# Kernel tuning notes

Hardware: AMD Instinct MI355X
Metric: run time of the kernel (lower is better)

## Reference

```python
import jax, jax.numpy as jnp
import numpy as np
import math

B, S, HID = 2, 2048, 2048
NH, NKV = 32, 8
HD = HID // NH  # 64
N_REP = NH // NKV  # 4


def setup_inputs() -> dict:
    key = jax.random.key(0)
    ks = jax.random.split(key, 7)
    sc = 0.02
    return {
        "hidden_states": jax.random.normal(ks[0], (B, S, HID), jnp.float32),
        "cos": jax.random.normal(ks[1], (S, HD), jnp.float32),
        "sin": jax.random.normal(ks[2], (S, HD), jnp.float32),
        "wq": jax.random.normal(ks[3], (NH * HD, HID), jnp.float32) * sc,
        "wk": jax.random.normal(ks[4], (NKV * HD, HID), jnp.float32) * sc,
        "wv": jax.random.normal(ks[5], (NKV * HD, HID), jnp.float32) * sc,
        "wo": jax.random.normal(ks[6], (HID, NH * HD), jnp.float32) * sc,
    }


def _rotate_half(x):
    x1, x2 = jnp.split(x, 2, axis=-1)
    return jnp.concatenate([-x2, x1], axis=-1)


def _apply_rotary(q, k, cos, sin):
    # q: [B,S,NH,HD], k: [B,S,NKV,HD]; cos/sin: [S,HD] broadcast over batch, heads
    c = cos[None, :, None, :]
    s = sin[None, :, None, :]
    return q * c + _rotate_half(q) * s, k * c + _rotate_half(k) * s


def reference(hidden_states, cos, sin, wq, wk, wv, wo):
    x = hidden_states  # [B,S,HID]
    q = jnp.einsum('bsh,dh->bsd', x, wq).reshape(B, S, NH, HD)
    k = jnp.einsum('bsh,dh->bsd', x, wk).reshape(B, S, NKV, HD)
    v = jnp.einsum('bsh,dh->bsd', x, wv).reshape(B, S, NKV, HD)
    q, k = _apply_rotary(q, k, cos, sin)
    # repeat_kv: expand kv heads by N_REP -> [B,S,NH,HD]
    k = jnp.repeat(k, N_REP, axis=2)
    v = jnp.repeat(v, N_REP, axis=2)
    # [B,NH,S,HD]
    q = q.transpose(0, 2, 1, 3)
    k = k.transpose(0, 2, 1, 3)
    v = v.transpose(0, 2, 1, 3)
    scores = jnp.einsum('bhqd,bhkd->bhqk', q, k) / math.sqrt(HD)
    probs = jax.nn.softmax(scores.astype(jnp.float32), axis=-1).astype(q.dtype)
    out = jnp.einsum('bhqk,bhkd->bhqd', probs, v)
    out = out.transpose(0, 2, 1, 3).reshape(B, S, NH * HD)
    return jnp.einsum('bsd,hd->bsh', out, wo)
```

## Files before the change

### kernel.cpp

```cpp
#include <hip/hip_runtime.h>
#include <math.h>

#define B 2
#define S 2048
#define HID 2048
#define NH 32
#define NKV 8
#define HD 64
#define NREP 4

typedef __bf16 bf16_t;
typedef bf16_t bf16x8 __attribute__((ext_vector_type(8)));
typedef bf16_t bf16x4 __attribute__((ext_vector_type(4)));
typedef bf16_t bf16x2 __attribute__((ext_vector_type(2)));
typedef float floatx4 __attribute__((ext_vector_type(4)));

__device__ __forceinline__ void gld_lds16(const void* g, void* l) {
    __builtin_amdgcn_global_load_lds(
        (const __attribute__((address_space(1))) void*)g,
        (__attribute__((address_space(3))) void*)l, 16, 0, 0);
}

__device__ __forceinline__ int pack2(float a, float b) {
    bf16x2 v; v[0] = (bf16_t)a; v[1] = (bf16_t)b;
    return __builtin_bit_cast(int, v);
}

__device__ __forceinline__ bf16x8 cat8i(int2 lo, int2 hi) {
    int4 w; w.x = lo.x; w.y = lo.y; w.z = hi.x; w.w = hi.y;
    return __builtin_bit_cast(bf16x8, w);
}

__global__ __launch_bounds__(256) void cast_all(const float* __restrict__ x,
                                                const float* __restrict__ wq,
                                                const float* __restrict__ wk,
                                                const float* __restrict__ wv,
                                                const float* __restrict__ wo,
                                                bf16_t* __restrict__ xb,
                                                bf16_t* __restrict__ wqkvb,
                                                bf16_t* __restrict__ wob) {
    int gid = blockIdx.x * 256 + threadIdx.x;
    const float* src; bf16_t* dst; int idx;
    if (gid < 1048576)      { src = x;  dst = xb;               idx = gid; }
    else if (gid < 1572864) { src = wq; dst = wqkvb;            idx = gid - 1048576; }
    else if (gid < 1703936) { src = wk; dst = wqkvb + 4194304;  idx = gid - 1572864; }
    else if (gid < 1835008) { src = wv; dst = wqkvb + 5242880;  idx = gid - 1703936; }
    else                    { src = wo; dst = wob;              idx = gid - 1835008; }
    size_t i = (size_t)idx * 8;
    float4 f0 = *(const float4*)(src + i);
    float4 f1 = *(const float4*)(src + i + 4);
    bf16x8 v;
    v[0] = (bf16_t)f0.x; v[1] = (bf16_t)f0.y; v[2] = (bf16_t)f0.z; v[3] = (bf16_t)f0.w;
    v[4] = (bf16_t)f1.x; v[5] = (bf16_t)f1.y; v[6] = (bf16_t)f1.z; v[7] = (bf16_t)f1.w;
    *(bf16x8*)(dst + i) = v;
}

#define TM 128
#define TN 128
#define BK 64

enum { MODE_QKV = 0, MODE_OUT = 2 };

template <int MODE>
__global__ __launch_bounds__(256) void gemm_mfma(const bf16_t* __restrict__ A,
                                                 const bf16_t* __restrict__ W,
                                                 void* __restrict__ outQ,
                                                 bf16_t* __restrict__ outK,
                                                 bf16_t* __restrict__ outV,
                                                 const float* __restrict__ cosp,
                                                 const float* __restrict__ sinp,
                                                 int M, int N, int K) {
    __shared__ __align__(16) bf16_t As[2 * TM * 32];
    __shared__ __align__(16) bf16_t Ws[2 * TN * 32];
    const int t    = threadIdx.x;
    const int wave = t >> 6, lane = t & 63;
    const int quad = lane >> 4, l16 = lane & 15;
    const int m0 = blockIdx.y * TM, n0 = blockIdx.x * TN;
    const int wm = (wave >> 1) * 64, wn = (wave & 1) * 64;

    floatx4 zero4 = {0.f, 0.f, 0.f, 0.f};
    floatx4 acc[4][4];
    #pragma unroll
    for (int i = 0; i < 4; ++i)
        #pragma unroll
        for (int j = 0; j < 4; ++j) acc[i][j] = zero4;

    const int r4 = t >> 2;
    const int c8 = (t & 3) * 8;
    const bf16_t* Arow = A + (size_t)(m0 + r4) * K + c8;
    const bf16_t* Wrow = W + (size_t)(n0 + r4) * K + c8;

    for (int k0 = 0; k0 < K; k0 += BK) {
        #pragma unroll
        for (int ks = 0; ks < 2; ++ks) {
            gld_lds16(Arow + k0 + ks * 32,          As + ks * 4096 + t * 8);
            gld_lds16(Arow + 64 * K + k0 + ks * 32, As + ks * 4096 + 2048 + t * 8);
            gld_lds16(Wrow + k0 + ks * 32,          Ws + ks * 4096 + t * 8);
            gld_lds16(Wrow + 64 * K + k0 + ks * 32, Ws + ks * 4096 + 2048 + t * 8);
        }
        __syncthreads();
        #pragma unroll
        for (int ks = 0; ks < 2; ++ks) {
            bf16x8 af[4], bfr[4];
            #pragma unroll
            for (int i = 0; i < 4; ++i)
                af[i] = *(bf16x8*)&As[ks * 4096 + (wm + i * 16 + l16) * 32 + quad * 8];
            #pragma unroll
            for (int j = 0; j < 4; ++j)
                bfr[j] = *(bf16x8*)&Ws[ks * 4096 + (wn + j * 16 + l16) * 32 + quad * 8];
            #pragma unroll
            for (int i = 0; i < 4; ++i)
                #pragma unroll
                for (int j = 0; j < 4; ++j)
                    acc[i][j] = __builtin_amdgcn_mfma_f32_16x16x32_bf16(af[i], bfr[j], acc[i][j], 0, 0, 0);
        }
        __syncthreads();
    }

    if constexpr (MODE == MODE_OUT) {
        float* C = (float*)outQ;
        #pragma unroll
        for (int i = 0; i < 4; ++i)
            #pragma unroll
            for (int r = 0; r < 4; ++r) {
                int row = m0 + wm + i * 16 + quad * 4 + r;
                #pragma unroll
                for (int j = 0; j < 4; ++j)
                    C[(size_t)row * N + n0 + wn + j * 16 + l16] = acc[i][j][r];
            }
    } else {
        const int hh = (n0 + wn) / 64;
        #pragma unroll
        for (int i = 0; i < 4; ++i)
            #pragma unroll
            for (int r = 0; r < 4; ++r) {
                int m = m0 + wm + i * 16 + quad * 4 + r;
                int b = m / S, s = m % S;
                if (hh < NH + NKV) {
                    bf16_t* base;
                    float sc;
                    if (hh < NH) {
                        base = (bf16_t*)outQ + ((size_t)(b * NH + hh) * S + s) * HD;
                        sc = 0.18033688011f;
                    } else {
                        base = outK + ((size_t)(b * NKV + (hh - NH)) * S + s) * HD;
                        sc = 1.0f;
                    }
                    #pragma unroll
                    for (int j = 0; j < 2; ++j) {
                        int d = j * 16 + l16;
                        float x1 = acc[i][j][r], x2 = acc[i][j + 2][r];
                        float c1 = cosp[s * HD + d],      s1 = sinp[s * HD + d];
                        float c2 = cosp[s * HD + d + 32], s2 = sinp[s * HD + d + 32];
                        base[d]      = (bf16_t)((x1 * c1 - x2 * s1) * sc);
                        base[d + 32] = (bf16_t)((x2 * c2 + x1 * s2) * sc);
                    }
                } else {
                    int kvh = hh - NH - NKV;
                    int w  = s & 63, lo = w & 31;
                    int pos = (lo < 16) ? (((lo >> 2) << 3) | (lo & 3))
                                        : ((((lo - 16) >> 2) << 3) | 4 | (lo & 3));
                    int ps = (s & ~63) | ((w & 32) + pos);
                    bf16_t* vb = outV + ((size_t)(b * NKV + kvh) * HD) * S + ps;
                    #pragma unroll
                    for (int j = 0; j < 4; ++j)
                        vb[(size_t)(j * 16 + l16) * S] = (bf16_t)acc[i][j][r];
                }
            }
    }
}

__global__ __launch_bounds__(256, 4) void attn_mfma(const bf16_t* __restrict__ Q,
                                                    const bf16_t* __restrict__ Kb,
                                                    const bf16_t* __restrict__ Vt,
                                                    bf16_t* __restrict__ Ob) {
    __shared__ __align__(16) bf16_t Ks[2 * 64 * 32];
    __shared__ __align__(16) bf16_t Vs[2 * 64 * 32];
    const int t    = threadIdx.x;
    const int wave = t >> 6, lane = t & 63;
    const int quad = lane >> 4, l16 = lane & 15;

    const int flat  = blockIdx.y * 16 + blockIdx.x;
    const int local = flat >> 3;
    const int combo = (flat & 7) * 2 + (local >> 6);
    const int b = combo >> 3, kvh = combo & 7;
    const int h  = kvh * NREP + ((local >> 4) & 3);
    const int q0 = (local & 15) * 128;
    const int bh = b * NH + h;

    const bf16_t* qbase = Q + ((size_t)bh * S + q0 + wave * 32) * HD;
    const bf16_t* kbase = Kb + ((size_t)(b * NKV + kvh) * S) * HD;
    const bf16_t* vbase = Vt + (size_t)(b * NKV + kvh) * HD * S;

    bf16x8 qf[2][2];
    #pragma unroll
    for (int qj = 0; qj < 2; ++qj)
        #pragma unroll
        for (int ks = 0; ks < 2; ++ks)
            qf[qj][ks] = *(const bf16x8*)(qbase + (size_t)(qj * 16 + l16) * HD + ks * 32 + quad * 8);

    floatx4 zero4 = {0.f, 0.f, 0.f, 0.f};
    floatx4 of[4][2];
    #pragma unroll
    for (int di = 0; di < 4; ++di)
        #pragma unroll
        for (int qj = 0; qj < 2; ++qj) of[di][qj] = zero4;
    float lsum[2] = {0.f, 0.f};

    const int r4 = t >> 2;
    const int c8 = (t & 3) * 8;

    #pragma unroll
    for (int ks = 0; ks < 2; ++ks)
        gld_lds16(kbase + (size_t)r4 * HD + ks * 32 + c8, Ks + ks * 2048 + t * 8);
    __syncthreads();

    for (int kt = 0; kt < S; kt += 64) {
        #pragma unroll
        for (int ks = 0; ks < 2; ++ks)
            gld_lds16(vbase + (size_t)r4 * S + kt + ks * 32 + c8, Vs + ks * 2048 + t * 8);

        int2 pk[4][2];
        #pragma unroll
        for (int ki = 0; ki < 4; ++ki) {
            bf16x8 ka0 = *(bf16x8*)&Ks[0 * 2048 + (ki * 16 + l16) * 32 + quad * 8];
            bf16x8 ka1 = *(bf16x8*)&Ks[1 * 2048 + (ki * 16 + l16) * 32 + quad * 8];
            floatx4 sf[2];
            #pragma unroll
            for (int qj = 0; qj < 2; ++qj) sf[qj] = zero4;
            __builtin_amdgcn_s_setprio(1);
            #pragma unroll
            for (int qj = 0; qj < 2; ++qj)
                sf[qj] = __builtin_amdgcn_mfma_f32_16x16x32_bf16(ka0, qf[qj][0], sf[qj], 0, 0, 0);
            #pragma unroll
            for (int qj = 0; qj < 2; ++qj)
                sf[qj] = __builtin_amdgcn_mfma_f32_16x16x32_bf16(ka1, qf[qj][1], sf[qj], 0, 0, 0);
            __builtin_amdgcn_s_setprio(0);
            #pragma unroll
            for (int qj = 0; qj < 2; ++qj) {
                float p0 = __builtin_amdgcn_exp2f(sf[qj][0]);
                float p1 = __builtin_amdgcn_exp2f(sf[qj][1]);
                float p2 = __builtin_amdgcn_exp2f(sf[qj][2]);
                float p3 = __builtin_amdgcn_exp2f(sf[qj][3]);
                lsum[qj] += (p0 + p1) + (p2 + p3);
                pk[ki][qj].x = pack2(p0, p1);
                pk[ki][qj].y = pack2(p2, p3);
            }
        }
        __syncthreads();

        if (kt + 64 < S) {
            #pragma unroll
            for (int ks = 0; ks < 2; ++ks)
                gld_lds16(kbase + (size_t)(kt + 64 + r4) * HD + ks * 32 + c8, Ks + ks * 2048 + t * 8);
        }
        #pragma unroll
        for (int ks = 0; ks < 2; ++ks) {
            __builtin_amdgcn_s_setprio(1);
            #pragma unroll
            for (int di = 0; di < 4; ++di) {
                bf16x8 va = *(bf16x8*)&Vs[ks * 2048 + (di * 16 + l16) * 32 + quad * 8];
                #pragma unroll
                for (int qj = 0; qj < 2; ++qj) {
                    bf16x8 pb = cat8i(pk[2 * ks][qj], pk[2 * ks + 1][qj]);
                    of[di][qj] = __builtin_amdgcn_mfma_f32_16x16x32_bf16(va, pb, of[di][qj], 0, 0, 0);
                }
            }
            __builtin_amdgcn_s_setprio(0);
        }
        __syncthreads();
    }

    #pragma unroll
    for (int qj = 0; qj < 2; ++qj) {
        float ls = lsum[qj];
        ls += __shfl_xor(ls, 16);
        ls += __shfl_xor(ls, 32);
        float inv = 1.f / ls;
        int q = q0 + wave * 32 + qj * 16 + l16;
        bf16_t* ob = Ob + ((size_t)(b * S + q)) * HID + h * HD;
        #pragma unroll
        for (int di = 0; di < 4; ++di) {
            int2 pkv;
            pkv.x = pack2(of[di][qj][0] * inv, of[di][qj][1] * inv);
            pkv.y = pack2(of[di][qj][2] * inv, of[di][qj][3] * inv);
            *(int2*)(ob + di * 16 + quad * 4) = pkv;
        }
    }
}

extern "C" void kernel_launch(void* const* d_in, const int* in_sizes, int n_in,
                              void* d_out, int out_size, void* d_ws, size_t ws_size,
                              hipStream_t stream) {
    const float* x    = (const float*)d_in[0];
    const float* cosp = (const float*)d_in[1];
    const float* sinp = (const float*)d_in[2];
    const float* wq   = (const float*)d_in[3];
    const float* wk   = (const float*)d_in[4];
    const float* wv   = (const float*)d_in[5];
    const float* wo   = (const float*)d_in[6];
    float* out = (float*)d_out;

    char* ws = (char*)d_ws;
    bf16_t* xb    = (bf16_t*)(ws);
    bf16_t* kb    = (bf16_t*)(ws + 16777216);
    bf16_t* vtb   = (bf16_t*)(ws + 20971520);
    bf16_t* wqkvb = (bf16_t*)(ws + 25165824);
    bf16_t* wob   = (bf16_t*)(ws + 37748736);
    bf16_t* attb  = (bf16_t*)(ws);
    bf16_t* qb    = (bf16_t*)d_out;

    const int M = B * S;

    cast_all<<<9216, 256, 0, stream>>>(x, wq, wk, wv, wo, xb, wqkvb, wob);

    gemm_mfma<MODE_QKV><<<dim3(3072 / TN, M / TM), 256, 0, stream>>>(
        xb, wqkvb, (void*)qb, kb, vtb, cosp, sinp, M, 3072, HID);

    attn_mfma<<<dim3(S / 128, B * NH), 256, 0, stream>>>(qb, kb, vtb, attb);

    gemm_mfma<MODE_OUT><<<dim3(2048 / TN, M / TM), 256, 0, stream>>>(
        attb, wob, (void*)out, nullptr, nullptr, nullptr, nullptr, M, 2048, HID);
}
```

Before: 305.8 us.

## Add 256x256-tile 8-wave QKV GEMM with staged LDS pipeline and fused RoPE

Replaces the 128x128 QKV projection GEMM with a new kernel that uses 256x256 output tiles, 512 threads (8 waves each computing 128x64), and double-buffered direct global-to-LDS loads interleaved with MFMA phases using s_setprio and barriers. The larger tile raises arithmetic intensity and cuts global loads per FLOP, and the fused epilogue still applies RoPE, scaling and the V transpose layout. The grid shrinks to 12x16 = 192 blocks, which can underfill the CUs, and the heavy register and LDS use limits occupancy.

```diff
diff --git a/kernel.cpp b/kernel.cpp
--- a/kernel.cpp
+++ b/kernel.cpp
@@ -53,6 +53,153 @@
     v[0] = (bf16_t)f0.x; v[1] = (bf16_t)f0.y; v[2] = (bf16_t)f0.z; v[3] = (bf16_t)f0.w;
     v[4] = (bf16_t)f1.x; v[5] = (bf16_t)f1.y; v[6] = (bf16_t)f1.z; v[7] = (bf16_t)f1.w;
     *(bf16x8*)(dst + i) = v;
+}
+
+__global__ __launch_bounds__(512, 2) void gemm8_qkv(const bf16_t* __restrict__ A,
+                                                    const bf16_t* __restrict__ W,
+                                                    bf16_t* __restrict__ outQ,
+                                                    bf16_t* __restrict__ outK,
+                                                    bf16_t* __restrict__ outV,
+                                                    const float* __restrict__ cosp,
+                                                    const float* __restrict__ sinp) {
+    __shared__ __align__(16) bf16_t As[2][2][256][32];
+    __shared__ __align__(16) bf16_t Bs[2][2][256][32];
+    const int t    = threadIdx.x;
+    const int wave = t >> 6, lane = t & 63;
+    const int quad = lane >> 4, l16 = lane & 15;
+    const int wm = (wave >> 2) * 128;
+    const int wn = (wave & 3) * 64;
+    const int m0 = blockIdx.y * 256, n0 = blockIdx.x * 256;
+    const int KK = HID;
+
+    floatx4 zero4 = {0.f, 0.f, 0.f, 0.f};
+    floatx4 acc[8][4];
+    #pragma unroll
+    for (int i = 0; i < 8; ++i)
+        #pragma unroll
+        for (int j = 0; j < 4; ++j) acc[i][j] = zero4;
+
+    const int sr = t >> 2, sc = (t & 3) * 8;
+    const bf16_t* Abase = A + (size_t)(m0 + sr) * KK + sc;
+    const bf16_t* Wbase = W + (size_t)(n0 + sr) * KK + sc;
+
+#define STAGE_A8(buf, kp, tt) do {                                          \
+        const bf16_t* g_ = Abase + (tt) * 64 + (kp) * 32;                   \
+        gld_lds16(g_,                 &As[buf][kp][0][0] + t * 8);          \
+        gld_lds16(g_ + 128 * KK,      &As[buf][kp][128][0] + t * 8);        \
+    } while (0)
+#define STAGE_B8(buf, kp, tt) do {                                          \
+        const bf16_t* g_ = Wbase + (tt) * 64 + (kp) * 32;                   \
+        gld_lds16(g_,                 &Bs[buf][kp][0][0] + t * 8);          \
+        gld_lds16(g_ + 128 * KK,      &Bs[buf][kp][128][0] + t * 8);        \
+    } while (0)
+#define LDA8(buf, kp, rf) (*(const bf16x8*)&As[buf][kp][wm + (rf) * 16 + l16][quad * 8])
+#define LDB8(buf, kp, cf) (*(const bf16x8*)&Bs[buf][kp][wn + (cf) * 16 + l16][quad * 8])
+#define MFMA16(rbase)                                                        \
+    __builtin_amdgcn_s_setprio(1);                                          \
+    _Pragma("unroll")                                                       \
+    for (int rf = 0; rf < 4; ++rf)                                          \
+        _Pragma("unroll")                                                   \
+        for (int cf = 0; cf < 4; ++cf)                                      \
+            acc[(rbase) + rf][cf] = __builtin_amdgcn_mfma_f32_16x16x32_bf16(\
+                af[rf], bfr[cf], acc[(rbase) + rf][cf], 0, 0, 0);           \
+    __builtin_amdgcn_s_setprio(0);
+
+    STAGE_A8(0, 0, 0); STAGE_B8(0, 0, 0);
+    STAGE_A8(0, 1, 0); STAGE_B8(0, 1, 0);
+    asm volatile("s_waitcnt vmcnt(4)" ::: "memory");
+    __builtin_amdgcn_s_barrier();
+
+    const int NT = KK / 64;
+    for (int tt = 0; tt < NT; ++tt) {
+        const int buf = tt & 1, nbuf = buf ^ 1;
+        const bool more = (tt + 1 < NT);
+        bf16x8 af[4], bfr[4];
+
+        #pragma unroll
+        for (int cf = 0; cf < 4; ++cf) bfr[cf] = LDB8(buf, 0, cf);
+        #pragma unroll
+        for (int rf = 0; rf < 4; ++rf) af[rf] = LDA8(buf, 0, rf);
+        if (more) STAGE_A8(nbuf, 0, tt + 1);
+        __builtin_amdgcn_s_barrier();
+        MFMA16(0);
+        __builtin_amdgcn_s_barrier();
+
+        #pragma unroll
+        for (int rf = 0; rf < 4; ++rf) af[rf] = LDA8(buf, 0, rf + 4);
+        if (more) {
+            STAGE_B8(nbuf, 0, tt + 1);
+            asm volatile("s_waitcnt vmcnt(4)" ::: "memory");
+        } else {
+            asm volatile("s_waitcnt vmcnt(0)" ::: "memory");
+        }
+        __builtin_amdgcn_s_barrier();
+        MFMA16(4);
+        __builtin_amdgcn_s_barrier();
+
+        #pragma unroll
+        for (int cf = 0; cf < 4; ++cf) bfr[cf] = LDB8(buf, 1, cf);
+        #pragma unroll
+        for (int rf = 0; rf < 4; ++rf) af[rf] = LDA8(buf, 1, rf);
+        if (more) STAGE_A8(nbuf, 1, tt + 1);
+        __builtin_amdgcn_s_barrier();
+        MFMA16(0);
+        __builtin_amdgcn_s_barrier();
+
+        #pragma unroll
+        for (int rf = 0; rf < 4; ++rf) af[rf] = LDA8(buf, 1, rf + 4);
+        if (more) {
+            STAGE_B8(nbuf, 1, tt + 1);
+            asm volatile("s_waitcnt vmcnt(4)" ::: "memory");
+        }
+        __builtin_amdgcn_s_barrier();
+        MFMA16(4);
+        __builtin_amdgcn_s_barrier();
+    }
+#undef STAGE_A8
+#undef STAGE_B8
+#undef LDA8
+#undef LDB8
+#undef MFMA16
+
+    const int hh = blockIdx.x * 4 + (wave & 3);
+    #pragma unroll
+    for (int rf = 0; rf < 8; ++rf)
+        #pragma unroll
+        for (int r = 0; r < 4; ++r) {
+            int m = m0 + wm + rf * 16 + quad * 4 + r;
+            int b = m / S, s = m % S;
+            if (hh < NH + NKV) {
+                bf16_t* base;
+                float sc2;
+                if (hh < NH) {
+                    base = outQ + ((size_t)(b * NH + hh) * S + s) * HD;
+                    sc2 = 0.18033688011f;
+                } else {
+                    base = outK + ((size_t)(b * NKV + (hh - NH)) * S + s) * HD;
+                    sc2 = 1.0f;
+                }
+                #pragma unroll
+                for (int j = 0; j < 2; ++j) {
+                    int d = j * 16 + l16;
+                    float x1 = acc[rf][j][r], x2 = acc[rf][j + 2][r];
+                    float c1 = cosp[s * HD + d],      s1 = sinp[s * HD + d];
+                    float c2 = cosp[s * HD + d + 32], s2 = sinp[s * HD + d + 32];
+                    base[d]      = (bf16_t)((x1 * c1 - x2 * s1) * sc2);
+                    base[d + 32] = (bf16_t)((x2 * c2 + x1 * s2) * sc2);
+                }
+            } else {
+                int kvh = hh - NH - NKV;
+                int w  = s & 63, lo = w & 31;
+                int pos = (lo < 16) ? (((lo >> 2) << 3) | (lo & 3))
+                                    : ((((lo - 16) >> 2) << 3) | 4 | (lo & 3));
+                int ps = (s & ~63) | ((w & 32) + pos);
+                bf16_t* vb = outV + ((size_t)(b * NKV + kvh) * HD) * S + ps;
+                #pragma unroll
+                for (int j = 0; j < 4; ++j)
+                    vb[(size_t)(j * 16 + l16) * S] = (bf16_t)acc[rf][j][r];
+            }
+        }
 }
 
 #define TM 128
@@ -314,8 +461,8 @@
 
     cast_all<<<9216, 256, 0, stream>>>(x, wq, wk, wv, wo, xb, wqkvb, wob);
 
-    gemm_mfma<MODE_QKV><<<dim3(3072 / TN, M / TM), 256, 0, stream>>>(
-        xb, wqkvb, (void*)qb, kb, vtb, cosp, sinp, M, 3072, HID);
+    gemm8_qkv<<<dim3(3072 / 256, M / 256), 512, 0, stream>>>(
+        xb, wqkvb, qb, kb, vtb, cosp, sinp);
 
     attn_mfma<<<dim3(S / 128, B * NH), 256, 0, stream>>>(qb, kb, vtb, attb);
 
```

Result: slower. 332.5 us (+8.7%).

## Share K/V tiles across all GQA heads in a 512-thread attention block

Applied to the files above, without the earlier changes.

Restructures the attention kernel so each 512-thread block covers all four query heads that share one KV head, with each wave handling 64 query rows of one head. Each K/V tile loaded into LDS is therefore reused by 4 heads instead of 1, cutting global K/V traffic and LDS fill work per unit of compute. The grid shrinks from 1024 to 256 blocks and per-wave register use roughly doubles (accumulators and P fragments), which may lower occupancy and leave fewer blocks to spread across CUs.

```diff
diff --git a/kernel.cpp b/kernel.cpp
--- a/kernel.cpp
+++ b/kernel.cpp
@@ -170,74 +170,71 @@
     }
 }
 
-__global__ __launch_bounds__(256, 4) void attn_mfma(const bf16_t* __restrict__ Q,
+__global__ __launch_bounds__(512, 2) void attn_mfma(const bf16_t* __restrict__ Q,
                                                     const bf16_t* __restrict__ Kb,
                                                     const bf16_t* __restrict__ Vt,
                                                     bf16_t* __restrict__ Ob) {
-    __shared__ __align__(16) bf16_t Ks[2 * 64 * 32];
-    __shared__ __align__(16) bf16_t Vs[2 * 64 * 32];
+    __shared__ __align__(16) bf16_t Ks[2][64][32];
+    __shared__ __align__(16) bf16_t Vs[2][64][32];
     const int t    = threadIdx.x;
     const int wave = t >> 6, lane = t & 63;
     const int quad = lane >> 4, l16 = lane & 15;
 
     const int flat  = blockIdx.y * 16 + blockIdx.x;
     const int local = flat >> 3;
-    const int combo = (flat & 7) * 2 + (local >> 6);
+    const int combo = (flat & 7) * 2 + (local >> 4);
     const int b = combo >> 3, kvh = combo & 7;
-    const int h  = kvh * NREP + ((local >> 4) & 3);
     const int q0 = (local & 15) * 128;
-    const int bh = b * NH + h;
-
-    const bf16_t* qbase = Q + ((size_t)bh * S + q0 + wave * 32) * HD;
+    const int h  = kvh * NREP + (wave & 3);
+    const int qw = q0 + (wave >> 2) * 64;
+
+    const bf16_t* qbase = Q + ((size_t)(b * NH + h) * S + qw) * HD;
     const bf16_t* kbase = Kb + ((size_t)(b * NKV + kvh) * S) * HD;
     const bf16_t* vbase = Vt + (size_t)(b * NKV + kvh) * HD * S;
 
-    bf16x8 qf[2][2];
+    bf16x8 qf[4][2];
     #pragma unroll
-    for (int qj = 0; qj < 2; ++qj)
+    for (int qj = 0; qj < 4; ++qj)
         #pragma unroll
         for (int ks = 0; ks < 2; ++ks)
             qf[qj][ks] = *(const bf16x8*)(qbase + (size_t)(qj * 16 + l16) * HD + ks * 32 + quad * 8);
 
     floatx4 zero4 = {0.f, 0.f, 0.f, 0.f};
-    floatx4 of[4][2];
+    floatx4 of[4][4];
     #pragma unroll
     for (int di = 0; di < 4; ++di)
         #pragma unroll
-        for (int qj = 0; qj < 2; ++qj) of[di][qj] = zero4;
-    float lsum[2] = {0.f, 0.f};
-
-    const int r4 = t >> 2;
-    const int c8 = (t & 3) * 8;
-
-    #pragma unroll
-    for (int ks = 0; ks < 2; ++ks)
-        gld_lds16(kbase + (size_t)r4 * HD + ks * 32 + c8, Ks + ks * 2048 + t * 8);
+        for (int qj = 0; qj < 4; ++qj) of[di][qj] = zero4;
+    float lsum[4] = {0.f, 0.f, 0.f, 0.f};
+
+    const int sp = t >> 8;
+    const int sr = (t >> 2) & 63;
+    const int sc = (t & 3) * 8;
+
+    gld_lds16(kbase + (size_t)sr * HD + sp * 32 + sc, (bf16_t*)Ks + t * 8);
     __syncthreads();
 
     for (int kt = 0; kt < S; kt += 64) {
-        #pragma unroll
-        for (int ks = 0; ks < 2; ++ks)
-            gld_lds16(vbase + (size_t)r4 * S + kt + ks * 32 + c8, Vs + ks * 2048 + t * 8);
-
-        int2 pk[4][2];
+        gld_lds16(vbase + (size_t)sr * S + kt + sp * 32 + sc, (bf16_t*)Vs + t * 8);
+
+        int2 pk[4][4];
         #pragma unroll
         for (int ki = 0; ki < 4; ++ki) {
-            bf16x8 ka0 = *(bf16x8*)&Ks[0 * 2048 + (ki * 16 + l16) * 32 + quad * 8];
-            bf16x8 ka1 = *(bf16x8*)&Ks[1 * 2048 + (ki * 16 + l16) * 32 + quad * 8];
-            floatx4 sf[2];
-            #pragma unroll
-            for (int qj = 0; qj < 2; ++qj) sf[qj] = zero4;
+            bf16x8 ka0 = *(bf16x8*)&Ks[0][ki * 16 + l16][quad * 8];
+            bf16x8 ka1 = *(bf16x8*)&Ks[1][ki * 16 + l16][quad * 8];
+            floatx4 sf[4];
+            #pragma unroll
+            for (int qj = 0; qj < 4; ++qj) sf[qj] = zero4;
             __builtin_amdgcn_s_setprio(1);
             #pragma unroll
-            for (int qj = 0; qj < 2; ++qj)
+            for (int qj = 0; qj < 4; ++qj)
                 sf[qj] = __builtin_amdgcn_mfma_f32_16x16x32_bf16(ka0, qf[qj][0], sf[qj], 0, 0, 0);
             #pragma unroll
-            for (int qj = 0; qj < 2; ++qj)
+            for (int qj = 0; qj < 4; ++qj)
                 sf[qj] = __builtin_amdgcn_mfma_f32_16x16x32_bf16(ka1, qf[qj][1], sf[qj], 0, 0, 0);
             __builtin_amdgcn_s_setprio(0);
             #pragma unroll
-            for (int qj = 0; qj < 2; ++qj) {
+            for (int qj = 0; qj < 4; ++qj) {
                 float p0 = __builtin_amdgcn_exp2f(sf[qj][0]);
                 float p1 = __builtin_amdgcn_exp2f(sf[qj][1]);
                 float p2 = __builtin_amdgcn_exp2f(sf[qj][2]);
@@ -249,19 +246,16 @@
         }
         __syncthreads();
 
-        if (kt + 64 < S) {
-            #pragma unroll
-            for (int ks = 0; ks < 2; ++ks)
-                gld_lds16(kbase + (size_t)(kt + 64 + r4) * HD + ks * 32 + c8, Ks + ks * 2048 + t * 8);
-        }
+        if (kt + 64 < S)
+            gld_lds16(kbase + (size_t)(kt + 64 + sr) * HD + sp * 32 + sc, (bf16_t*)Ks + t * 8);
         #pragma unroll
         for (int ks = 0; ks < 2; ++ks) {
             __builtin_amdgcn_s_setprio(1);
             #pragma unroll
             for (int di = 0; di < 4; ++di) {
-                bf16x8 va = *(bf16x8*)&Vs[ks * 2048 + (di * 16 + l16) * 32 + quad * 8];
+                bf16x8 va = *(bf16x8*)&Vs[ks][di * 16 + l16][quad * 8];
                 #pragma unroll
-                for (int qj = 0; qj < 2; ++qj) {
+                for (int qj = 0; qj < 4; ++qj) {
                     bf16x8 pb = cat8i(pk[2 * ks][qj], pk[2 * ks + 1][qj]);
                     of[di][qj] = __builtin_amdgcn_mfma_f32_16x16x32_bf16(va, pb, of[di][qj], 0, 0, 0);
                 }
@@ -272,12 +266,12 @@
     }
 
     #pragma unroll
-    for (int qj = 0; qj < 2; ++qj) {
+    for (int qj = 0; qj < 4; ++qj) {
         float ls = lsum[qj];
         ls += __shfl_xor(ls, 16);
         ls += __shfl_xor(ls, 32);
         float inv = 1.f / ls;
-        int q = q0 + wave * 32 + qj * 16 + l16;
+        int q = qw + qj * 16 + l16;
         bf16_t* ob = Ob + ((size_t)(b * S + q)) * HID + h * HD;
         #pragma unroll
         for (int di = 0; di < 4; ++di) {
@@ -317,7 +311,7 @@
     gemm_mfma<MODE_QKV><<<dim3(3072 / TN, M / TM), 256, 0, stream>>>(
         xb, wqkvb, (void*)qb, kb, vtb, cosp, sinp, M, 3072, HID);
 
-    attn_mfma<<<dim3(S / 128, B * NH), 256, 0, stream>>>(qb, kb, vtb, attb);
+    attn_mfma<<<dim3(16, 16), 512, 0, stream>>>(qb, kb, vtb, attb);
 
     gemm_mfma<MODE_OUT><<<dim3(2048 / TN, M / TM), 256, 0, stream>>>(
         attb, wob, (void*)out, nullptr, nullptr, nullptr, nullptr, M, 2048, HID);
```

New measurement: 310.1 us. No clear change (+1.4%).
